# Optimization experiments

Hardware: AMD Instinct MI355X
Metric: run time of the kernel (lower is better)

Reference implementation:

```python
import jax, jax.numpy as jnp
import numpy as np

L, K, D, V, S, B = 2, 4, 1024, 32000, 1024, 2

# Constant neighbor influence from the 2x2 grid (success_rate==0.5 for fresh blocks)
_pos = np.array([[0, 0], [0, 1], [1, 0], [1, 1]], dtype=np.float64)
_dist = np.sqrt(((_pos[:, None, :] - _pos[None, :, :]) ** 2).sum(-1))
_infl = np.where(np.eye(K, dtype=bool), 0.0, 0.5 / (1.0 + _dist)).sum(-1)
NEIGHBOR_SIG = jnp.asarray(1.0 / (1.0 + np.exp(-_infl)), dtype=jnp.float32)  # [K]


def _ln(x, g, b, eps=1e-5):
    mu = x.mean(-1, keepdims=True)
    var = ((x - mu) ** 2).mean(-1, keepdims=True)
    return (x - mu) / jnp.sqrt(var + eps) * g + b


def setup_inputs() -> dict:
    key = jax.random.key(0)
    ks = jax.random.split(key, 10)
    def n(k, shape, s):
        return jax.random.normal(k, shape, jnp.float32) * s
    return {
        "input_ids": jax.random.randint(ks[0], (B, S), 0, V),
        "embedding": n(ks[1], (V, D), 0.02),
        "pos_enc": n(ks[2], (S, D), 0.02),
        "torsion_field": jnp.zeros((D,), jnp.float32),
        "ln1_g": jnp.ones((L, D), jnp.float32),
        "ln1_b": jnp.zeros((L, D), jnp.float32),
        "base_W": n(ks[3], (L, D, D), 0.02),
        "blk_W1": n(ks[4], (L, K, D // 2, D), 0.02),
        "blk_W2": n(ks[5], (L, K, D, D // 2), 0.02),
        "blk_gate": n(ks[6], (L, K, D), 0.01),
        "prop_W": n(ks[7], (L, K, K), 0.5),
        "prop_b": jnp.zeros((L, K), jnp.float32),
        "ln2_g": jnp.ones((L, D), jnp.float32),
        "ln2_b": jnp.zeros((L, D), jnp.float32),
        "out_ln_g": jnp.ones((D,), jnp.float32),
        "out_ln_b": jnp.zeros((D,), jnp.float32),
        "lm_head_W": n(ks[8], (V, D), 0.02),
    }


def reference(input_ids, embedding, pos_enc, torsion_field, ln1_g, ln1_b,
              base_W, blk_W1, blk_W2, blk_gate, prop_W, prop_b,
              ln2_g, ln2_b, out_ln_g, out_ln_b, lm_head_W):
    h = embedding[input_ids] + pos_enc[None]  # [B,S,D]
    s = jnp.full((K,), 0.5, h.dtype)  # fresh blocks: success_rate = 0.5
    for l in range(L):
        # excitement (detached in torch via .item())
        exc0 = jax.nn.sigmoid(prop_W[l] @ s + prop_b[l])
        exc = jax.lax.stop_gradient(0.6 * exc0 + 0.4 * NEIGHBOR_SIG)  # [K]
        hn = _ln(h, ln1_g[l], ln1_b[l])
        base = hn @ base_W[l].T  # [B,S,D]
        # all K blocks are always loaded (min_blocks == max_blocks == 4)
        t = jnp.einsum('bsd,khd->bksh', hn, blk_W1[l])
        t = jax.nn.gelu(t, approximate=False)
        t = jnp.einsum('bksh,kdh->bksd', t, blk_W2[l])
        gate = jax.nn.sigmoid(blk_gate[l] + torsion_field)  # [K,D]
        t = t * gate[None, :, None, :]
        combined = jnp.einsum('bksd,k->bsd', t, exc) / exc.sum()
        h = h + (base + combined) * 0.3
        h = _ln(h, ln2_g[l], ln2_b[l])
    h = _ln(h, out_ln_g, out_ln_b)
    return h @ lm_head_W.T  # [B,S,V]
```

## Files before the change

### kernel.cpp

```cpp
#include <hip/hip_runtime.h>
#include <math.h>

typedef unsigned short u16;
typedef short s16x8 __attribute__((ext_vector_type(8)));
typedef float f32x4 __attribute__((ext_vector_type(4)));
typedef u16 u16x4 __attribute__((ext_vector_type(4)));

#define D 1024
#define MM 2048
#define HH 512
#define VV 32000

static __device__ __forceinline__ u16 f2bf(float f) {
    union { float f; unsigned int i; } c; c.f = f;
    unsigned int x = c.i;
    return (u16)((x + 0x7fffu + ((x >> 16) & 1u)) >> 16);
}
static __device__ __forceinline__ float sigm(float x) { return 1.0f / (1.0f + expf(-x)); }

static __device__ __forceinline__ void load_lds16(const u16* g, u16* l) {
    __builtin_amdgcn_global_load_lds(
        (const __attribute__((address_space(1))) unsigned int*)g,
        (__attribute__((address_space(3))) unsigned int*)l, 16, 0, 0);
}

__global__ __launch_bounds__(256) void cvt_kernel(const float* __restrict__ in,
                                                  u16* __restrict__ out, const int n4)
{
    for (int i = blockIdx.x * 256 + threadIdx.x; i < n4; i += gridDim.x * 256) {
        f32x4 v = __builtin_nontemporal_load((const f32x4*)in + i);
        u16x4 o;
#pragma unroll
        for (int j = 0; j < 4; j++) o[j] = f2bf(v[j]);
        ((u16x4*)out)[i] = o;
    }
}

__global__ __launch_bounds__(256) void cvtcat_kernel(const float* __restrict__ baseW,
    const float* __restrict__ W1, u16* __restrict__ out)
{
    const int N4 = 3072 * 1024 / 4, B4 = 1024 * 1024 / 4;
    for (int i = blockIdx.x * 256 + threadIdx.x; i < N4; i += gridDim.x * 256) {
        f32x4 v = (i < B4) ? __builtin_nontemporal_load((const f32x4*)baseW + i)
                           : __builtin_nontemporal_load((const f32x4*)W1 + (i - B4));
        u16x4 o;
#pragma unroll
        for (int j = 0; j < 4; j++) o[j] = f2bf(v[j]);
        ((u16x4*)out)[i] = o;
    }
}

__global__ __launch_bounds__(256) void embed_ln_kernel(const int* __restrict__ ids,
    const float* __restrict__ emb, const float* __restrict__ pos,
    const float* __restrict__ g, const float* __restrict__ b,
    float* __restrict__ h, u16* __restrict__ hn)
{
    const int m = blockIdx.x;
    const int s = m & 1023;
    const long id = ids[m];
    const int d = threadIdx.x * 4;
    f32x4 ev = *(const f32x4*)&emb[id * D + d];
    f32x4 pv = *(const f32x4*)&pos[(long)s * D + d];
    f32x4 x;
#pragma unroll
    for (int i = 0; i < 4; i++) x[i] = ev[i] + pv[i];
    *(f32x4*)&h[(long)m * D + d] = x;

    float sm = x[0] + x[1] + x[2] + x[3];
    float ss = x[0]*x[0] + x[1]*x[1] + x[2]*x[2] + x[3]*x[3];
#pragma unroll
    for (int off = 32; off; off >>= 1) { sm += __shfl_xor(sm, off); ss += __shfl_xor(ss, off); }
    __shared__ float red[8];
    const int wid = threadIdx.x >> 6;
    if ((threadIdx.x & 63) == 0) { red[wid] = sm; red[4 + wid] = ss; }
    __syncthreads();
    sm = red[0] + red[1] + red[2] + red[3];
    ss = red[4] + red[5] + red[6] + red[7];
    const float mu = sm * (1.0f / D);
    const float rstd = rsqrtf(ss * (1.0f / D) - mu * mu + 1e-5f);
    f32x4 gv = *(const f32x4*)&g[d];
    f32x4 bv = *(const f32x4*)&b[d];
    u16x4 o;
#pragma unroll
    for (int i = 0; i < 4; i++) o[i] = f2bf((x[i] - mu) * rstd * gv[i] + bv[i]);
    *(u16x4*)&hn[(long)m * D + d] = o;
}

__global__ __launch_bounds__(256) void resln2_kernel(float* __restrict__ h,
    const float* __restrict__ c, const float* __restrict__ g2, const float* __restrict__ b2,
    const float* __restrict__ gn, const float* __restrict__ bn_, u16* __restrict__ hn)
{
    const int row = blockIdx.x;
    const int d = threadIdx.x * 4;
    f32x4 x = *(const f32x4*)&h[(long)row * D + d];
    f32x4 cv = *(const f32x4*)&c[(long)row * D + d];
#pragma unroll
    for (int i = 0; i < 4; i++) x[i] += 0.3f * cv[i];
    float sm = x[0] + x[1] + x[2] + x[3];
    float ss = x[0]*x[0] + x[1]*x[1] + x[2]*x[2] + x[3]*x[3];
#pragma unroll
    for (int off = 32; off; off >>= 1) { sm += __shfl_xor(sm, off); ss += __shfl_xor(ss, off); }
    __shared__ float red[8];
    const int wid = threadIdx.x >> 6;
    if ((threadIdx.x & 63) == 0) { red[wid] = sm; red[4 + wid] = ss; }
    __syncthreads();
    sm = red[0] + red[1] + red[2] + red[3];
    ss = red[4] + red[5] + red[6] + red[7];
    float mu = sm * (1.0f / D);
    float rstd = rsqrtf(ss * (1.0f / D) - mu * mu + 1e-5f);
    f32x4 g2v = *(const f32x4*)&g2[d];
    f32x4 b2v = *(const f32x4*)&b2[d];
    f32x4 y;
#pragma unroll
    for (int i = 0; i < 4; i++) y[i] = (x[i] - mu) * rstd * g2v[i] + b2v[i];
    *(f32x4*)&h[(long)row * D + d] = y;

    sm = y[0] + y[1] + y[2] + y[3];
    ss = y[0]*y[0] + y[1]*y[1] + y[2]*y[2] + y[3]*y[3];
#pragma unroll
    for (int off = 32; off; off >>= 1) { sm += __shfl_xor(sm, off); ss += __shfl_xor(ss, off); }
    __syncthreads();
    if ((threadIdx.x & 63) == 0) { red[wid] = sm; red[4 + wid] = ss; }
    __syncthreads();
    sm = red[0] + red[1] + red[2] + red[3];
    ss = red[4] + red[5] + red[6] + red[7];
    mu = sm * (1.0f / D);
    rstd = rsqrtf(ss * (1.0f / D) - mu * mu + 1e-5f);
    f32x4 gnv = *(const f32x4*)&gn[d];
    f32x4 bnv = *(const f32x4*)&bn_[d];
    u16x4 o;
#pragma unroll
    for (int i = 0; i < 4; i++) o[i] = f2bf((y[i] - mu) * rstd * gnv[i] + bnv[i]);
    *(u16x4*)&hn[(long)row * D + d] = o;
}

__global__ __launch_bounds__(256) void scale_w2x_kernel(
    const float* __restrict__ W2l, const float* __restrict__ gatel,
    const float* __restrict__ tors, const float* __restrict__ pW,
    const float* __restrict__ pb, u16* __restrict__ W2eff)
{
    const float NS = 1.0f / (1.0f + expf(-0.70710678118654752f));
    float e[4], sum = 0.0f;
#pragma unroll
    for (int k = 0; k < 4; k++) {
        float a = pb[k] + 0.5f * (pW[k*4] + pW[k*4+1] + pW[k*4+2] + pW[k*4+3]);
        e[k] = 0.6f * sigm(a) + 0.4f * NS;
        sum += e[k];
    }
    const int n = blockIdx.x >> 1;
    const int half = blockIdx.x & 1;
    const int kh = half * 1024 + threadIdx.x * 4;
    const int k = kh >> 9;
    const int hh = kh & 511;
    const float f = sigm(gatel[k * D + n] + tors[n]) * (e[k] / sum);
    f32x4 w = __builtin_nontemporal_load((const f32x4*)&W2l[((long)k * D + n) * HH + hh]);
    u16x4 o;
#pragma unroll
    for (int i = 0; i < 4; i++) o[i] = f2bf(w[i] * f);
    *(u16x4*)&W2eff[(long)n * 2048 + kh] = o;
}

template<int EPI>
__global__ __launch_bounds__(256) void gemm_t(
    const u16* __restrict__ A, const u16* __restrict__ W,
    float* __restrict__ Cf, u16* __restrict__ Cb,
    const int Kloop, const int ldk, const long ldc)
{
    if (EPI == 4) { A += blockIdx.z * 512; W += blockIdx.z * 512; }

    const int gx = gridDim.x;
    const int nwg = gx * gridDim.y;
    int lin = blockIdx.y * gx + blockIdx.x;
    lin = (lin & 7) * (nwg >> 3) + (lin >> 3);
    const int bm = (lin % gx) * 128;
    const int bn = (lin / gx) * 128;

    __shared__ __align__(16) u16 AB[8192];

    const int tid = threadIdx.x, lane = tid & 63, w = tid >> 6;
    const int wm = w >> 1, wn = w & 1;
    const int l15 = lane & 15, lk8 = (lane >> 4) * 8;

    const u16* src[4];
    u16* dst[4];
#pragma unroll
    for (int ci = 0; ci < 4; ++ci) {
        const int c = w + ci * 4;
        src[ci] = (c < 8 ? A + (long)(bm + c * 16 + l15) * ldk
                         : W + (long)(bn + (c - 8) * 16 + l15) * ldk) + lk8;
        dst[ci] = AB + c * 512;
    }

    f32x4 acc[4][4];
#pragma unroll
    for (int i = 0; i < 4; ++i)
#pragma unroll
        for (int j = 0; j < 4; ++j) acc[i][j] = f32x4{0.f, 0.f, 0.f, 0.f};

    for (int k0 = 0; k0 < Kloop; k0 += 32) {
        __syncthreads();
#pragma unroll
        for (int ci = 0; ci < 4; ++ci) load_lds16(src[ci] + k0, dst[ci]);
        __syncthreads();
        s16x8 a[4], b[4];
#pragma unroll
        for (int i = 0; i < 4; ++i) a[i] = *(const s16x8*)(AB + (wm * 4 + i) * 512 + lane * 8);
#pragma unroll
        for (int j = 0; j < 4; ++j) b[j] = *(const s16x8*)(AB + (8 + wn * 4 + j) * 512 + lane * 8);
#pragma unroll
        for (int i = 0; i < 4; ++i)
#pragma unroll
            for (int j = 0; j < 4; ++j)
                acc[i][j] = __builtin_amdgcn_mfma_f32_16x16x32_bf16(a[i], b[j], acc[i][j], 0, 0, 0);
    }

    const int r0 = (lane >> 4) * 4;
#pragma unroll
    for (int i = 0; i < 4; ++i) {
#pragma unroll
        for (int j = 0; j < 4; ++j) {
            const int n = bn + wn * 64 + j * 16 + l15;
#pragma unroll
            for (int rr = 0; rr < 4; ++rr) {
                const int m = bm + wm * 64 + i * 16 + r0 + rr;
                const float v = acc[i][j][rr];
                if (EPI == 3) {
                    if (n < 1024) {
                        Cf[(long)m * 1024 + n] = v;
                    } else {
                        const float gel = 0.5f * v * (1.0f + erff(v * 0.70710678118654752f));
                        Cb[(long)m * 2048 + (n - 1024)] = f2bf(gel);
                    }
                } else {
                    atomicAdd(&Cf[(long)m * ldc + n], v);
                }
            }
        }
    }
}

#define AU16  16384
#define HALFU 8192
#define BB0   32768

__global__ __launch_bounds__(512, 2) void gemm256_kernel(
    const u16* __restrict__ Ag, const u16* __restrict__ Wg, float* __restrict__ C)
{
    __shared__ __align__(16) u16 lds[65536];

    const int nwg = gridDim.x * gridDim.y;
    int lin = blockIdx.y * gridDim.x + blockIdx.x;
    lin = (lin & 7) * (nwg >> 3) + (lin >> 3);
    const int bm = (lin & 7) * 256;
    const int bn = (lin >> 3) * 256;

    const int tid = threadIdx.x;
    const int lane = tid & 63;
    const int w = tid >> 6;
    const int wm = w >> 2;
    const int wn = w & 3;

    const u16* aSrc = Ag + (long)(bm + w * 16 + (lane & 15)) * 1024 + ((lane >> 4) * 8);
    const u16* bSrc = Wg + (long)(bn + w * 16 + (lane & 15)) * 1024 + ((lane >> 4) * 8);
    u16* aDst = lds + w * 1024;
    u16* bDst = lds + BB0 + w * 1024;

    auto stageA = [&](int kt, int b, int kk) {
        const long co = (long)kt * 64 + kk * 32;
        load_lds16(aSrc + co,               aDst + b * AU16 + kk * 512);
        load_lds16(aSrc + co + 128 * 1024L, aDst + b * AU16 + HALFU + kk * 512);
    };
    auto stageB = [&](int kt, int b, int kk) {
        const long co = (long)kt * 64 + kk * 32;
        load_lds16(bSrc + co,               bDst + b * AU16 + kk * 512);
        load_lds16(bSrc + co + 128 * 1024L, bDst + b * AU16 + HALFU + kk * 512);
    };

    const u16* aRd = lds + wm * HALFU + lane * 8;
    const u16* bRd = lds + BB0 + (wn >> 1) * HALFU + (wn & 1) * 4096 + lane * 8;

    f32x4 acc[8][4];
#pragma unroll
    for (int i = 0; i < 8; ++i)
#pragma unroll
        for (int j = 0; j < 4; ++j) acc[i][j] = f32x4{0.f, 0.f, 0.f, 0.f};

    s16x8 F0[12], F1[12];

    stageA(0, 0, 0); stageB(0, 0, 0);
    stageA(0, 0, 1); stageB(0, 0, 1);
    stageA(1, 1, 0); stageB(1, 1, 0);
    asm volatile("s_waitcnt vmcnt(4)" ::: "memory");
    __builtin_amdgcn_s_barrier();
    __builtin_amdgcn_sched_barrier(0);

#pragma unroll
    for (int i = 0; i < 8; ++i) F0[i] = *(const s16x8*)(aRd + i * 1024);
#pragma unroll
    for (int j = 0; j < 4; ++j) F0[8 + j] = *(const s16x8*)(bRd + j * 1024);

    auto phase = [&](int p, s16x8 (&fu)[12], s16x8 (&fl)[12]) {
        const int pr = p + 1;
        const int Tr = (pr >> 1) & 15, kkr = pr & 1, br = Tr & 1;
        const u16* aR = aRd + br * AU16 + kkr * 512;
        const u16* bR = bRd + br * AU16 + kkr * 512;
#pragma unroll
        for (int i = 0; i < 8; ++i) fl[i] = *(const s16x8*)(aR + i * 1024);
#pragma unroll
        for (int j = 0; j < 4; ++j) fl[8 + j] = *(const s16x8*)(bR + j * 1024);
        const int us = 6 + 2 * p;
        const int Ts = (us >> 2) & 15, kks = (us >> 1) & 1, bs = Ts & 1;
        stageA(Ts, bs, kks);
        stageB(Ts, bs, kks);
        __builtin_amdgcn_sched_barrier(0);
        __builtin_amdgcn_s_setprio(1);
#pragma unroll
        for (int j = 0; j < 4; ++j)
#pragma unroll
            for (int i = 0; i < 8; ++i)
                acc[i][j] = __builtin_amdgcn_mfma_f32_16x16x32_bf16(fu[i], fu[8 + j], acc[i][j], 0, 0, 0);
        __builtin_amdgcn_s_setprio(0);
        __builtin_amdgcn_sched_barrier(0);
        asm volatile("s_waitcnt vmcnt(4)" ::: "memory");
        __builtin_amdgcn_s_barrier();
        __builtin_amdgcn_sched_barrier(0);
    };

    for (int p = 0; p < 32; p += 2) {
        phase(p,     F0, F1);
        phase(p + 1, F1, F0);
    }

    asm volatile("s_waitcnt vmcnt(0)" ::: "memory");

    const int r0 = (lane >> 4) * 4;
    const int cl = lane & 15;
#pragma unroll
    for (int i = 0; i < 8; ++i)
#pragma unroll
        for (int j = 0; j < 4; ++j) {
            const long m = bm + wm * 128 + i * 16 + r0;
            const int n = bn + wn * 64 + j * 16 + cl;
#pragma unroll
            for (int rr = 0; rr < 4; ++rr)
                C[(m + rr) * (long)VV + n] = acc[i][j][rr];
        }
}

extern "C" void kernel_launch(void* const* d_in, const int* in_sizes, int n_in,
                              void* d_out, int out_size, void* d_ws, size_t ws_size,
                              hipStream_t stream)
{
    (void)in_sizes; (void)n_in; (void)out_size; (void)ws_size;
    const int*   ids   = (const int*)d_in[0];
    const float* emb   = (const float*)d_in[1];
    const float* pos   = (const float*)d_in[2];
    const float* tors  = (const float*)d_in[3];
    const float* ln1g  = (const float*)d_in[4];
    const float* ln1b  = (const float*)d_in[5];
    const float* baseW = (const float*)d_in[6];
    const float* W1    = (const float*)d_in[7];
    const float* W2    = (const float*)d_in[8];
    const float* gate  = (const float*)d_in[9];
    const float* propW = (const float*)d_in[10];
    const float* propb = (const float*)d_in[11];
    const float* ln2g  = (const float*)d_in[12];
    const float* ln2b  = (const float*)d_in[13];
    const float* outg  = (const float*)d_in[14];
    const float* outb  = (const float*)d_in[15];
    const float* lmW   = (const float*)d_in[16];

    char* ws = (char*)d_ws;
    float* h     = (float*)(ws);
    u16*   hn    = (u16*)  (ws + (8l  << 20));
    u16*   Wcat  = (u16*)  (ws + (12l << 20));
    float* C     = (float*)(ws + (18l << 20));
    u16*   t     = (u16*)  (ws + (26l << 20));
    u16*   W2eff = (u16*)  (ws + (34l << 20));
    u16*   lmWbf = (u16*)  (ws + (12l << 20));

    embed_ln_kernel<<<MM, 256, 0, stream>>>(ids, emb, pos, ln1g, ln1b, h, hn);

    for (int l = 0; l < 2; l++) {
        cvtcat_kernel<<<1024, 256, 0, stream>>>(
            baseW + (long)l * D * D, W1 + (long)l * 4 * HH * D, Wcat);
        scale_w2x_kernel<<<2048, 256, 0, stream>>>(
            W2 + (long)l * 4 * D * HH, gate + (long)l * 4 * D, tors,
            propW + l * 16, propb + l * 4, W2eff);
        gemm_t<3><<<dim3(16, 24), 256, 0, stream>>>(hn, Wcat, C, t, 1024, 1024, 0);
        gemm_t<4><<<dim3(16, 8, 4), 256, 0, stream>>>(t, W2eff, C, nullptr, 512, 2048, 1024);
        resln2_kernel<<<MM, 256, 0, stream>>>(
            h, C, ln2g + (long)l * D, ln2b + (long)l * D,
            l == 0 ? ln1g + D : outg, l == 0 ? ln1b + D : outb, hn);
    }

    cvt_kernel<<<2048, 256, 0, stream>>>(lmW, lmWbf, VV * D / 4);
    gemm256_kernel<<<dim3(8, 125), 512, 0, stream>>>(hn, lmWbf, (float*)d_out);
}
```

Baseline: 421.1 us.

## Fuse lm_head fp32-to-bf16 conversion into GEMM and merge weight prep kernels

The separate cvt_kernel that converted the 32000x1024 fp32 lm_head weight to bf16 is removed. The final GEMM now loads fp32 B tiles into registers, converts them and writes them to LDS inside a reworked software pipeline. This saves a full write and re-read of the bf16 weight copy. Separately, cvtcat and scale_w2x are merged into one prep_kernel launch per layer. The trade-off is that each of the 8 M-tile blocks now re-reads and re-converts fp32 B, doubling B global traffic per block, and register-staged B loads add pressure and latency to the pipeline.

```diff
diff --git a/kernel.cpp b/kernel.cpp
--- a/kernel.cpp
+++ b/kernel.cpp
@@ -5,6 +5,7 @@
 typedef short s16x8 __attribute__((ext_vector_type(8)));
 typedef float f32x4 __attribute__((ext_vector_type(4)));
 typedef u16 u16x4 __attribute__((ext_vector_type(4)));
+typedef u16 u16x8 __attribute__((ext_vector_type(8)));
 
 #define D 1024
 #define MM 2048
@@ -23,31 +24,11 @@
         (const __attribute__((address_space(1))) unsigned int*)g,
         (__attribute__((address_space(3))) unsigned int*)l, 16, 0, 0);
 }
-
-__global__ __launch_bounds__(256) void cvt_kernel(const float* __restrict__ in,
-                                                  u16* __restrict__ out, const int n4)
-{
-    for (int i = blockIdx.x * 256 + threadIdx.x; i < n4; i += gridDim.x * 256) {
-        f32x4 v = __builtin_nontemporal_load((const f32x4*)in + i);
-        u16x4 o;
-#pragma unroll
-        for (int j = 0; j < 4; j++) o[j] = f2bf(v[j]);
-        ((u16x4*)out)[i] = o;
-    }
-}
-
-__global__ __launch_bounds__(256) void cvtcat_kernel(const float* __restrict__ baseW,
-    const float* __restrict__ W1, u16* __restrict__ out)
-{
-    const int N4 = 3072 * 1024 / 4, B4 = 1024 * 1024 / 4;
-    for (int i = blockIdx.x * 256 + threadIdx.x; i < N4; i += gridDim.x * 256) {
-        f32x4 v = (i < B4) ? __builtin_nontemporal_load((const f32x4*)baseW + i)
-                           : __builtin_nontemporal_load((const f32x4*)W1 + (i - B4));
-        u16x4 o;
-#pragma unroll
-        for (int j = 0; j < 4; j++) o[j] = f2bf(v[j]);
-        ((u16x4*)out)[i] = o;
-    }
+static __device__ __forceinline__ u16x8 cvt8(f32x4 a, f32x4 b) {
+    u16x8 o;
+    o[0] = f2bf(a[0]); o[1] = f2bf(a[1]); o[2] = f2bf(a[2]); o[3] = f2bf(a[3]);
+    o[4] = f2bf(b[0]); o[5] = f2bf(b[1]); o[6] = f2bf(b[2]); o[7] = f2bf(b[3]);
+    return o;
 }
 
 __global__ __launch_bounds__(256) void embed_ln_kernel(const int* __restrict__ ids,
@@ -134,30 +115,47 @@
     *(u16x4*)&hn[(long)row * D + d] = o;
 }
 
-__global__ __launch_bounds__(256) void scale_w2x_kernel(
+__global__ __launch_bounds__(256) void prep_kernel(
+    const float* __restrict__ baseW, const float* __restrict__ W1,
     const float* __restrict__ W2l, const float* __restrict__ gatel,
     const float* __restrict__ tors, const float* __restrict__ pW,
-    const float* __restrict__ pb, u16* __restrict__ W2eff)
-{
-    const float NS = 1.0f / (1.0f + expf(-0.70710678118654752f));
-    float e[4], sum = 0.0f;
-#pragma unroll
-    for (int k = 0; k < 4; k++) {
-        float a = pb[k] + 0.5f * (pW[k*4] + pW[k*4+1] + pW[k*4+2] + pW[k*4+3]);
-        e[k] = 0.6f * sigm(a) + 0.4f * NS;
-        sum += e[k];
-    }
-    const int n = blockIdx.x >> 1;
-    const int half = blockIdx.x & 1;
-    const int kh = half * 1024 + threadIdx.x * 4;
-    const int k = kh >> 9;
-    const int hh = kh & 511;
-    const float f = sigm(gatel[k * D + n] + tors[n]) * (e[k] / sum);
-    f32x4 w = __builtin_nontemporal_load((const f32x4*)&W2l[((long)k * D + n) * HH + hh]);
-    u16x4 o;
-#pragma unroll
-    for (int i = 0; i < 4; i++) o[i] = f2bf(w[i] * f);
-    *(u16x4*)&W2eff[(long)n * 2048 + kh] = o;
+    const float* __restrict__ pb, u16* __restrict__ Wcat, u16* __restrict__ W2eff)
+{
+    int bid = blockIdx.x;
+    if (bid < 1024) {
+        const int B4 = 1024 * 1024 / 4;
+#pragma unroll
+        for (int it = 0; it < 3; ++it) {
+            const int i = (it * 1024 + bid) * 256 + threadIdx.x;
+            f32x4 v = (i < B4) ? __builtin_nontemporal_load((const f32x4*)baseW + i)
+                               : __builtin_nontemporal_load((const f32x4*)W1 + (i - B4));
+            u16x4 o;
+#pragma unroll
+            for (int j = 0; j < 4; j++) o[j] = f2bf(v[j]);
+            ((u16x4*)Wcat)[i] = o;
+        }
+    } else {
+        bid -= 1024;
+        const float NS = 1.0f / (1.0f + expf(-0.70710678118654752f));
+        float e[4], sum = 0.0f;
+#pragma unroll
+        for (int k = 0; k < 4; k++) {
+            float a = pb[k] + 0.5f * (pW[k*4] + pW[k*4+1] + pW[k*4+2] + pW[k*4+3]);
+            e[k] = 0.6f * sigm(a) + 0.4f * NS;
+            sum += e[k];
+        }
+        const int n = bid >> 1;
+        const int half = bid & 1;
+        const int kh = half * 1024 + threadIdx.x * 4;
+        const int k = kh >> 9;
+        const int hh = kh & 511;
+        const float f = sigm(gatel[k * D + n] + tors[n]) * (e[k] / sum);
+        f32x4 w = __builtin_nontemporal_load((const f32x4*)&W2l[((long)k * D + n) * HH + hh]);
+        u16x4 o;
+#pragma unroll
+        for (int i = 0; i < 4; i++) o[i] = f2bf(w[i] * f);
+        *(u16x4*)&W2eff[(long)n * 2048 + kh] = o;
+    }
 }
 
 template<int EPI>
@@ -243,8 +241,8 @@
 #define HALFU 8192
 #define BB0   32768
 
-__global__ __launch_bounds__(512, 2) void gemm256_kernel(
-    const u16* __restrict__ Ag, const u16* __restrict__ Wg, float* __restrict__ C)
+__global__ __launch_bounds__(512, 2) void gemm256f_kernel(
+    const u16* __restrict__ Ag, const float* __restrict__ Wf, float* __restrict__ C)
 {
     __shared__ __align__(16) u16 lds[65536];
 
@@ -254,31 +252,48 @@
     const int bm = (lin & 7) * 256;
     const int bn = (lin >> 3) * 256;
 
-    const int tid = threadIdx.x;
-    const int lane = tid & 63;
-    const int w = tid >> 6;
-    const int wm = w >> 2;
-    const int wn = w & 3;
-
-    const u16* aSrc = Ag + (long)(bm + w * 16 + (lane & 15)) * 1024 + ((lane >> 4) * 8);
-    const u16* bSrc = Wg + (long)(bn + w * 16 + (lane & 15)) * 1024 + ((lane >> 4) * 8);
+    const int tid = threadIdx.x, lane = tid & 63, w = tid >> 6;
+    const int wm = w >> 2, wn = w & 3;
+
+    const u16*  aSrc  = Ag + (long)(bm + w * 16 + (lane & 15)) * 1024 + ((lane >> 4) * 8);
+    const float* bSrcF = Wf + (long)(bn + w * 16 + (lane & 15)) * 1024 + ((lane >> 4) * 8);
     u16* aDst = lds + w * 1024;
-    u16* bDst = lds + BB0 + w * 1024;
-
-    auto stageA = [&](int kt, int b, int kk) {
-        const long co = (long)kt * 64 + kk * 32;
+    u16* bWr  = lds + BB0 + w * 1024 + lane * 8;
+
+    auto stageA = [&](int q) {
+        const int T = (q >> 1) & 15, b = (q >> 1) & 1, kk = q & 1;
+        const long co = (long)T * 64 + kk * 32;
         load_lds16(aSrc + co,               aDst + b * AU16 + kk * 512);
         load_lds16(aSrc + co + 128 * 1024L, aDst + b * AU16 + HALFU + kk * 512);
     };
-    auto stageB = [&](int kt, int b, int kk) {
-        const long co = (long)kt * 64 + kk * 32;
-        load_lds16(bSrc + co,               bDst + b * AU16 + kk * 512);
-        load_lds16(bSrc + co + 128 * 1024L, bDst + b * AU16 + HALFU + kk * 512);
+    auto issueB = [&](int q, f32x4 (&r)[4]) {
+        const int T = (q >> 1) & 15, kk = q & 1;
+        const long co = (long)T * 64 + kk * 32;
+        r[0] = *(const f32x4*)(bSrcF + co);
+        r[1] = *(const f32x4*)(bSrcF + co + 4);
+        r[2] = *(const f32x4*)(bSrcF + co + 128 * 1024L);
+        r[3] = *(const f32x4*)(bSrcF + co + 128 * 1024L + 4);
+    };
+    auto writeB = [&](int q, f32x4 (&r)[4]) {
+        const int b = (q >> 1) & 1, kk = q & 1;
+        u16* wd = bWr + b * AU16 + kk * 512;
+        *(u16x8*)wd = cvt8(r[0], r[1]);
+        *(u16x8*)(wd + HALFU) = cvt8(r[2], r[3]);
     };
 
     const u16* aRd = lds + wm * HALFU + lane * 8;
     const u16* bRd = lds + BB0 + (wn >> 1) * HALFU + (wn & 1) * 4096 + lane * 8;
 
+    auto fragRead = [&](int q, s16x8 (&F)[12]) {
+        const int b = (q >> 1) & 1, kk = q & 1;
+        const u16* aR = aRd + b * AU16 + kk * 512;
+        const u16* bR = bRd + b * AU16 + kk * 512;
+#pragma unroll
+        for (int i = 0; i < 8; ++i) F[i] = *(const s16x8*)(aR + i * 1024);
+#pragma unroll
+        for (int j = 0; j < 4; ++j) F[8 + j] = *(const s16x8*)(bR + j * 1024);
+    };
+
     f32x4 acc[8][4];
 #pragma unroll
     for (int i = 0; i < 8; ++i)
@@ -286,32 +301,30 @@
         for (int j = 0; j < 4; ++j) acc[i][j] = f32x4{0.f, 0.f, 0.f, 0.f};
 
     s16x8 F0[12], F1[12];
-
-    stageA(0, 0, 0); stageB(0, 0, 0);
-    stageA(0, 0, 1); stageB(0, 0, 1);
-    stageA(1, 1, 0); stageB(1, 1, 0);
-    asm volatile("s_waitcnt vmcnt(4)" ::: "memory");
+    f32x4 b0[4], b1[4], t0[4], t1[4];
+
+    issueB(0, t0); __builtin_amdgcn_sched_barrier(0);
+    stageA(0);     __builtin_amdgcn_sched_barrier(0);
+    issueB(1, t1); __builtin_amdgcn_sched_barrier(0);
+    stageA(1);     __builtin_amdgcn_sched_barrier(0);
+    issueB(2, b0); __builtin_amdgcn_sched_barrier(0);
+    stageA(2);     __builtin_amdgcn_sched_barrier(0);
+    issueB(3, b1); __builtin_amdgcn_sched_barrier(0);
+    asm volatile("s_waitcnt vmcnt(10)" ::: "memory");
+    writeB(0, t0);
+    writeB(1, t1);
+    asm volatile("s_waitcnt lgkmcnt(0)" ::: "memory");
     __builtin_amdgcn_s_barrier();
     __builtin_amdgcn_sched_barrier(0);
-
-#pragma unroll
-    for (int i = 0; i < 8; ++i) F0[i] = *(const s16x8*)(aRd + i * 1024);
-#pragma unroll
-    for (int j = 0; j < 4; ++j) F0[8 + j] = *(const s16x8*)(bRd + j * 1024);
-
-    auto phase = [&](int p, s16x8 (&fu)[12], s16x8 (&fl)[12]) {
-        const int pr = p + 1;
-        const int Tr = (pr >> 1) & 15, kkr = pr & 1, br = Tr & 1;
-        const u16* aR = aRd + br * AU16 + kkr * 512;
-        const u16* bR = bRd + br * AU16 + kkr * 512;
-#pragma unroll
-        for (int i = 0; i < 8; ++i) fl[i] = *(const s16x8*)(aR + i * 1024);
-#pragma unroll
-        for (int j = 0; j < 4; ++j) fl[8 + j] = *(const s16x8*)(bR + j * 1024);
-        const int us = 6 + 2 * p;
-        const int Ts = (us >> 2) & 15, kks = (us >> 1) & 1, bs = Ts & 1;
-        stageA(Ts, bs, kks);
-        stageB(Ts, bs, kks);
+    fragRead(0, F0);
+
+    auto phase = [&](int p, s16x8 (&fu)[12], s16x8 (&fl)[12], f32x4 (&bs)[4]) {
+        stageA(p + 3);
+        __builtin_amdgcn_sched_barrier(0);
+        asm volatile("s_waitcnt vmcnt(8)" ::: "memory");
+        fragRead(p + 1, fl);
+        writeB(p + 2, bs);
+        issueB(p + 4, bs);
         __builtin_amdgcn_sched_barrier(0);
         __builtin_amdgcn_s_setprio(1);
 #pragma unroll
@@ -321,14 +334,14 @@
                 acc[i][j] = __builtin_amdgcn_mfma_f32_16x16x32_bf16(fu[i], fu[8 + j], acc[i][j], 0, 0, 0);
         __builtin_amdgcn_s_setprio(0);
         __builtin_amdgcn_sched_barrier(0);
-        asm volatile("s_waitcnt vmcnt(4)" ::: "memory");
+        asm volatile("s_waitcnt lgkmcnt(0)" ::: "memory");
         __builtin_amdgcn_s_barrier();
         __builtin_amdgcn_sched_barrier(0);
     };
 
     for (int p = 0; p < 32; p += 2) {
-        phase(p,     F0, F1);
-        phase(p + 1, F1, F0);
+        phase(p,     F0, F1, b0);
+        phase(p + 1, F1, F0, b1);
     }
 
     asm volatile("s_waitcnt vmcnt(0)" ::: "memory");
@@ -377,16 +390,14 @@
     float* C     = (float*)(ws + (18l << 20));
     u16*   t     = (u16*)  (ws + (26l << 20));
     u16*   W2eff = (u16*)  (ws + (34l << 20));
-    u16*   lmWbf = (u16*)  (ws + (12l << 20));
 
     embed_ln_kernel<<<MM, 256, 0, stream>>>(ids, emb, pos, ln1g, ln1b, h, hn);
 
     for (int l = 0; l < 2; l++) {
-        cvtcat_kernel<<<1024, 256, 0, stream>>>(
-            baseW + (long)l * D * D, W1 + (long)l * 4 * HH * D, Wcat);
-        scale_w2x_kernel<<<2048, 256, 0, stream>>>(
+        prep_kernel<<<3072, 256, 0, stream>>>(
+            baseW + (long)l * D * D, W1 + (long)l * 4 * HH * D,
             W2 + (long)l * 4 * D * HH, gate + (long)l * 4 * D, tors,
-            propW + l * 16, propb + l * 4, W2eff);
+            propW + l * 16, propb + l * 4, Wcat, W2eff);
         gemm_t<3><<<dim3(16, 24), 256, 0, stream>>>(hn, Wcat, C, t, 1024, 1024, 0);
         gemm_t<4><<<dim3(16, 8, 4), 256, 0, stream>>>(t, W2eff, C, nullptr, 512, 2048, 1024);
         resln2_kernel<<<MM, 256, 0, stream>>>(
@@ -394,6 +405,5 @@
             l == 0 ? ln1g + D : outg, l == 0 ? ln1b + D : outb, hn);
     }
 
-    cvt_kernel<<<2048, 256, 0, stream>>>(lmW, lmWbf, VV * D / 4);
-    gemm256_kernel<<<dim3(8, 125), 512, 0, stream>>>(hn, lmWbf, (float*)d_out);
-}
+    gemm256f_kernel<<<dim3(8, 125), 512, 0, stream>>>(hn, lmW, (float*)d_out);
+}
```

New measurement: 716.4 us. +70.1%, slower.
